# Kernel tuning notes

Hardware: AMD Instinct MI355X
Metric: run time of the kernel (lower is better)

Reference implementation:

```python
import jax, jax.numpy as jnp
import numpy as np

# Kernel offset table copied VERBATIM from the source (note the duplicated
# [-1,-1] row where [-1,1] would be expected -- we replicate the bug).
OFF = jnp.array([[-1, -1], [-1, 0], [-1, -1], [0, -1], [0, 0], [0, 1],
                 [1, -1], [1, 0], [1, 1]], dtype=jnp.float32)  # (9, 2)

T_HARD = 3.14 / 6
S_HARD = 2.0
S_RANGE = (S_HARD - 1.0 / S_HARD) / 2.0
H_VEC = jnp.array([T_HARD, S_RANGE, S_RANGE], dtype=jnp.float32)
B_VEC = jnp.array([0.0, S_RANGE, S_RANGE], dtype=jnp.float32)
BN_EPS = 1e-5


def setup_inputs() -> dict:
    key = jax.random.key(0)
    ks = jax.random.split(key, 9)
    N, C, H, W, O = 8, 128, 64, 64, 128
    return {
        "input_feat": jax.random.normal(ks[0], (N, C, H, W), jnp.float32),
        "ste_w": 0.05 * jax.random.normal(ks[1], (3, C, 1, 1), jnp.float32),
        "ste_b": 0.05 * jax.random.normal(ks[2], (3,), jnp.float32),
        "bn_gamma": 1.0 + 0.1 * jax.random.normal(ks[3], (3,), jnp.float32),
        "bn_beta": 0.1 * jax.random.normal(ks[4], (3,), jnp.float32),
        "bn_mean": 0.1 * jax.random.normal(ks[5], (3,), jnp.float32),
        "bn_var": jax.random.uniform(ks[6], (3,), jnp.float32, 0.5, 1.5),
        "dconv_w": jax.random.normal(ks[7], (O, C, 3, 3), jnp.float32) / np.sqrt(C * 9.0),
        "dconv_b": 0.05 * jax.random.normal(ks[8], (O,), jnp.float32),
    }


def _forward(input_feat, ste_w, ste_b, bn_gamma, bn_beta, bn_mean, bn_var,
             dconv_w, dconv_b):
    N, C, H, W = input_feat.shape
    O = dconv_w.shape[0]
    # --- ste: 1x1 conv -> BatchNorm (eval) -> tanh, then affine H*x + B ---
    s = jnp.einsum('nchw,oc->nohw', input_feat, ste_w[:, :, 0, 0])
    s = s + ste_b[None, :, None, None]
    scale = (bn_gamma / jnp.sqrt(bn_var + BN_EPS))
    s = (s - bn_mean[None, :, None, None]) * scale[None, :, None, None] \
        + bn_beta[None, :, None, None]
    info = jnp.tanh(s) * H_VEC[None, :, None, None] + B_VEC[None, :, None, None]
    # --- per-pixel 2x2 scaled rotation applied to kernel grid ---
    theta = info[:, 0]                  # [N,H,W]
    sin = jnp.sin(theta)
    cos = jnp.cos(theta)
    a00 = cos * info[:, 1]
    a11 = cos * info[:, 2]
    awt = jnp.stack([a00, -sin, sin, a11], axis=-1).reshape(N, H, W, 2, 2)
    offs = jnp.einsum('kd,nhwde->nkhwe', OFF, awt)   # [N,9,H,W,2]
    off_y = offs[..., 0]
    off_x = offs[..., 1]
    # --- deformable 3x3 conv, stride 1, padding 1, zero-pad bilinear ---
    k = jnp.arange(9)
    dy = (k // 3 - 1).astype(jnp.float32)  # default kernel y-offsets
    dx = (k % 3 - 1).astype(jnp.float32)
    yy = jnp.arange(H, dtype=jnp.float32)
    xx = jnp.arange(W, dtype=jnp.float32)
    y = yy[None, None, :, None] + dy[None, :, None, None] + off_y  # [N,9,H,W]
    x = xx[None, None, None, :] + dx[None, :, None, None] + off_x
    y0 = jnp.floor(y)
    x0 = jnp.floor(x)
    wy = y - y0
    wx = x - x0
    y0i = y0.astype(jnp.int32)
    x0i = x0.astype(jnp.int32)

    def gather(img, yi, xi):
        # img [C,H,W], yi/xi [9,H,W] -> [C,9,H,W], zero outside bounds
        valid = (yi >= 0) & (yi < H) & (xi >= 0) & (xi < W)
        v = img[:, jnp.clip(yi, 0, H - 1), jnp.clip(xi, 0, W - 1)]
        return v * valid[None].astype(img.dtype)

    def sample_one(img, y0i, x0i, wy, wx):
        v00 = gather(img, y0i, x0i)
        v01 = gather(img, y0i, x0i + 1)
        v10 = gather(img, y0i + 1, x0i)
        v11 = gather(img, y0i + 1, x0i + 1)
        return (v00 * ((1 - wy) * (1 - wx))[None]
                + v01 * ((1 - wy) * wx)[None]
                + v10 * (wy * (1 - wx))[None]
                + v11 * (wy * wx)[None])

    samp = jax.vmap(sample_one)(input_feat, y0i, x0i, wy, wx)  # [N,C,9,H,W]
    out = jnp.einsum('nckhw,ock->nohw', samp, dconv_w.reshape(O, C, 9))
    return out + dconv_b[None, :, None, None]


def reference(input_feat, ste_w, ste_b, bn_gamma, bn_beta, bn_mean, bn_var,
              dconv_w, dconv_b):
    return _forward(input_feat, ste_w, ste_b, bn_gamma, bn_beta, bn_mean,
                    bn_var, dconv_w, dconv_b)
```

## Files before the change

### kernel.cpp

```cpp
#include <hip/hip_runtime.h>
#include <hip/hip_bf16.h>

constexpr int kN = 8, kC = 128, kH = 64, kW = 64, kO = 128;
constexpr int kHW = kH * kW;

typedef float f32x2 __attribute__((ext_vector_type(2)));
typedef float f32x4 __attribute__((ext_vector_type(4)));
typedef short bf16x8 __attribute__((ext_vector_type(8)));
typedef unsigned short ushort8 __attribute__((ext_vector_type(8)));
typedef unsigned int u32x4 __attribute__((ext_vector_type(4)));

__device__ __forceinline__ float bf2f(unsigned short u) {
  unsigned int x = ((unsigned int)u) << 16;
  return __builtin_bit_cast(float, x);
}
__device__ __forceinline__ unsigned short f2bf(float f) {
  unsigned int b = __builtin_bit_cast(unsigned int, f);
  b += 0x7FFFu + ((b >> 16) & 1u);
  return (unsigned short)(b >> 16);
}
__device__ __forceinline__ f32x2 bf2x2(unsigned int u) {
  f32x2 r;
  r[0] = __builtin_bit_cast(float, u << 16);
  r[1] = __builtin_bit_cast(float, u & 0xFFFF0000u);
  return r;
}

#define GLOAD_LDS16(g, l)                                              \
  __builtin_amdgcn_global_load_lds(                                    \
      (const __attribute__((address_space(1))) void*)(g),              \
      (__attribute__((address_space(3))) void*)(l), 16, 0, 0)

__global__ __launch_bounds__(256) void prep_kernel(
    const float* __restrict__ inp, const float* __restrict__ ste_w,
    const float* __restrict__ ste_b, const float* __restrict__ bn_g,
    const float* __restrict__ bn_b, const float* __restrict__ bn_m,
    const float* __restrict__ bn_v, unsigned short* __restrict__ nhwc,
    float* __restrict__ prm, const float* __restrict__ dw,
    unsigned short* __restrict__ wkb) {
  const int bid = blockIdx.x;
  if (bid >= kN * kH) {
    int idx = (bid - kN * kH) * 256 + threadIdx.x;
    if (idx < 9 * kO * kC) {
      int k = idx / (kO * kC);
      int r = idx - k * (kO * kC);
      int o = r >> 7, c = r & 127;
      int c8 = c >> 3;
      int dstc = ((c8 ^ (o & 7)) << 3) | (c & 7);
      wkb[k * (kO * kC) + (o << 7) + dstc] = f2bf(dw[(o * kC + c) * 9 + k]);
    }
    return;
  }

  __shared__ __align__(16) float tile[kC * kW];
  __shared__ float part[16][3][kW];
  const int tid = threadIdx.x;
  const int nh = bid;
  const int n = nh >> 6, h = nh & 63;
  const float* base = inp + (size_t)n * kC * kHW + h * kW;

  const int w4 = tid & 15;
  const int m = tid >> 4;
  float p0[4] = {0.f, 0.f, 0.f, 0.f};
  float p1[4] = {0.f, 0.f, 0.f, 0.f};
  float p2[4] = {0.f, 0.f, 0.f, 0.f};
#pragma unroll
  for (int it = 0; it < 8; ++it) {
    const int c = m + it * 16;
    f32x4 v = *(const f32x4*)(base + c * kHW + w4 * 4);
    ((f32x4*)tile)[c * 16 + (w4 ^ ((c >> 3) & 7))] = v;
    const float s0 = ste_w[c], s1 = ste_w[kC + c], s2 = ste_w[2 * kC + c];
#pragma unroll
    for (int e = 0; e < 4; ++e) {
      p0[e] += s0 * v[e];
      p1[e] += s1 * v[e];
      p2[e] += s2 * v[e];
    }
  }
#pragma unroll
  for (int e = 0; e < 4; ++e) {
    part[m][0][w4 * 4 + e] = p0[e];
    part[m][1][w4 * 4 + e] = p1[e];
    part[m][2][w4 * 4 + e] = p2[e];
  }
  __syncthreads();

  if (tid < kW) {
    const int w = tid;
    float s0 = 0.f, s1 = 0.f, s2 = 0.f;
#pragma unroll
    for (int g = 0; g < 16; ++g) {
      s0 += part[g][0][w];
      s1 += part[g][1][w];
      s2 += part[g][2][w];
    }
    s0 = (s0 + ste_b[0] - bn_m[0]) * (bn_g[0] * rsqrtf(bn_v[0] + 1e-5f)) + bn_b[0];
    s1 = (s1 + ste_b[1] - bn_m[1]) * (bn_g[1] * rsqrtf(bn_v[1] + 1e-5f)) + bn_b[1];
    s2 = (s2 + ste_b[2] - bn_m[2]) * (bn_g[2] * rsqrtf(bn_v[2] + 1e-5f)) + bn_b[2];
    float th = tanhf(s0) * (3.14f / 6.0f);
    float i1 = tanhf(s1) * 0.75f + 0.75f;
    float i2 = tanhf(s2) * 0.75f + 0.75f;
    float sn = sinf(th), cs = cosf(th);
    prm[nh * 192 + w * 3 + 0] = cs * i1;
    prm[nh * 192 + w * 3 + 1] = sn;
    prm[nh * 192 + w * 3 + 2] = cs * i2;
  }

#pragma unroll
  for (int it = 0; it < 4; ++it) {
    int i = tid + it * 256;
    int ch = i & 15, w = i >> 4;
    int c0 = ch * 8;
    const int xw = (((w >> 2) ^ (ch & 7)) << 2) + (w & 3);
    ushort8 v;
#pragma unroll
    for (int j = 0; j < 8; ++j) v[j] = f2bf(tile[(c0 + j) * kW + xw]);
    *(ushort8*)&nhwc[((size_t)(n * kH + h) * kW + w) * kC + c0] = v;
  }
}

__global__ __launch_bounds__(512, 4) void deform_mfma_kernel(
    const unsigned short* __restrict__ nhwc,
    const unsigned short* __restrict__ wkb,
    const float* __restrict__ prm, const float* __restrict__ db,
    float* __restrict__ out) {
  __shared__ __align__(16) unsigned short As[2][32 * 128];
  __shared__ __align__(16) unsigned short Bs[2][128 * 128];

  const int tid = threadIdx.x;
  const int lane = tid & 63, wave = tid >> 6;
  const int wid = (blockIdx.x & 7) * 128 + (blockIdx.x >> 3);
  const int nh = wid >> 1;
  const int w0 = (wid & 1) << 5;
  const int n = nh >> 6, h = nh & 63;
  const unsigned short* nhwc_n = nhwc + (size_t)n * kH * kW * kC;

  const int p = tid >> 4, ch = tid & 15;
  const int cb = ch * 8;
  const float a00 = prm[nh * 192 + (w0 + p) * 3 + 0];
  const float sn  = prm[nh * 192 + (w0 + p) * 3 + 1];
  const float a11 = prm[nh * 192 + (w0 + p) * 3 + 2];

  const int mg = wave >> 2, ng = wave & 3;
  const int row = mg * 16 + (lane & 15);
  const int kq = lane >> 4;
  const int rsw = (row & 7) << 4;
  f32x4 acc[2];
  acc[0] = (f32x4){0.f, 0.f, 0.f, 0.f};
  acc[1] = (f32x4){0.f, 0.f, 0.f, 0.f};

  u32x4 aC[4];
  float wgt[4];

  auto issue_B = [&](int k, int buf) {
    const char* gk = (const char*)wkb + (size_t)k * 32768;
    char* lb = (char*)Bs[buf];
    const int wo = wave * 1024;
    const int lo16 = lane * 16;
#pragma unroll
    for (int it = 0; it < 4; ++it) {
      GLOAD_LDS16(gk + it * 8192 + wo + lo16, lb + it * 8192 + wo);
    }
  };

  auto gather_A = [&](int k) {
    const float fdy = (float)(k / 3 - 1);
    const float fdx = (float)(k % 3 - 1);
    const float o0 = fdy;
    const float o1 = (k == 2) ? -1.0f : fdx;
    float y = (float)h + fdy + o0 * a00 + o1 * sn;
    float x = (float)(w0 + p) + fdx - o0 * sn + o1 * a11;
    float y0f = floorf(y), x0f = floorf(x);
    float wy = y - y0f, wx = x - x0f;
    int y0 = (int)y0f, x0 = (int)x0f;
    bool yv0 = (unsigned)y0 < (unsigned)kH;
    bool yv1 = (unsigned)(y0 + 1) < (unsigned)kH;
    bool xv0 = (unsigned)x0 < (unsigned)kW;
    bool xv1 = (unsigned)(x0 + 1) < (unsigned)kW;
    int y0c = min(max(y0, 0), kH - 1);
    int y1c = min(max(y0 + 1, 0), kH - 1);
    int x0c = min(max(x0, 0), kW - 1);
    int x1c = min(max(x0 + 1, 0), kW - 1);
    wgt[0] = (1.f - wy) * (1.f - wx) * (yv0 && xv0 ? 1.f : 0.f);
    wgt[1] = (1.f - wy) * wx * (yv0 && xv1 ? 1.f : 0.f);
    wgt[2] = wy * (1.f - wx) * (yv1 && xv0 ? 1.f : 0.f);
    wgt[3] = wy * wx * (yv1 && xv1 ? 1.f : 0.f);
    aC[0] = *(const u32x4*)&nhwc_n[((y0c * kW) + x0c) * kC + cb];
    aC[1] = *(const u32x4*)&nhwc_n[((y0c * kW) + x1c) * kC + cb];
    aC[2] = *(const u32x4*)&nhwc_n[((y1c * kW) + x0c) * kC + cb];
    aC[3] = *(const u32x4*)&nhwc_n[((y1c * kW) + x1c) * kC + cb];
  };

  auto write_A = [&](int buf) {
    u32x4 r;
#pragma unroll
    for (int t = 0; t < 4; ++t) {
      f32x2 v = bf2x2(aC[0][t]) * wgt[0] + bf2x2(aC[1][t]) * wgt[1] +
                bf2x2(aC[2][t]) * wgt[2] + bf2x2(aC[3][t]) * wgt[3];
      __hip_bfloat162 pk = __float22bfloat162_rn(float2{v[0], v[1]});
      unsigned int bits;
      __builtin_memcpy(&bits, &pk, 4);
      r[t] = bits;
    }
    *(u32x4*)((char*)As[buf] + p * 256 + ((ch * 16) ^ ((p & 7) << 4))) = r;
  };

  issue_B(0, 0);
  gather_A(0);
  write_A(0);
  __syncthreads();

  for (int k = 0; k < 9; ++k) {
    const int cur = k & 1;
    if (k < 8) {
      gather_A(k + 1);
      issue_B(k + 1, cur ^ 1);
    }

    const char* Ab = (const char*)As[cur] + row * 256;
    const char* Bb = (const char*)Bs[cur];
#pragma unroll
    for (int ks = 0; ks < 4; ++ks) {
      const int kb = ks * 64 + kq * 16;
      bf16x8 a = *(const bf16x8*)(Ab + (kb ^ rsw));
#pragma unroll
      for (int f = 0; f < 2; ++f) {
        const int orow = (ng * 2 + f) * 16 + (lane & 15);
        bf16x8 b = *(const bf16x8*)(Bb + orow * 256 + (kb ^ ((orow & 7) << 4)));
        acc[f] = __builtin_amdgcn_mfma_f32_16x16x32_bf16(a, b, acc[f], 0, 0, 0);
      }
    }

    if (k < 8) write_A(cur ^ 1);
    __syncthreads();
  }

  const int pixb = mg * 16 + (lane >> 4) * 4;
#pragma unroll
  for (int f = 0; f < 2; ++f) {
    const int o = (ng * 2 + f) * 16 + (lane & 15);
    const float bias = db[o];
    float4 v = {acc[f][0] + bias, acc[f][1] + bias, acc[f][2] + bias,
                acc[f][3] + bias};
    *(float4*)&out[((size_t)(n * kO + o)) * kHW + h * kW + w0 + pixb] = v;
  }
}

__global__ __launch_bounds__(256) void deform_kernel_f32(
    const float* __restrict__ inp, const float* __restrict__ ste_w,
    const float* __restrict__ ste_b, const float* __restrict__ bn_g,
    const float* __restrict__ bn_b, const float* __restrict__ bn_m,
    const float* __restrict__ bn_v, const float* __restrict__ dw,
    const float* __restrict__ db, float* __restrict__ out) {
  __shared__ __align__(16) float smp[kC * 16];
  __shared__ float prm[16][3];
  const int tid = threadIdx.x;
  const int base = blockIdx.x * 16;
  const int n = base / kHW;
  const int hw = base - n * kHW;
  const int h = hw / kW;
  const int w0 = hw - h * kW;
  const float* inp_n = inp + (size_t)n * kC * kHW;

  for (int i = tid; i < kC * 16; i += 256) {
    int c = i >> 4, p = i & 15;
    smp[i] = inp_n[c * kHW + h * kW + w0 + p];
  }
  __syncthreads();
  {
    const int p = tid >> 4, cl = tid & 15;
    float a0 = 0.f, a1 = 0.f, a2 = 0.f;
#pragma unroll
    for (int i = 0; i < 8; ++i) {
      int c = cl + (i << 4);
      float v = smp[c * 16 + p];
      a0 += v * ste_w[c];
      a1 += v * ste_w[kC + c];
      a2 += v * ste_w[2 * kC + c];
    }
#pragma unroll
    for (int off = 8; off; off >>= 1) {
      a0 += __shfl_down(a0, off, 16);
      a1 += __shfl_down(a1, off, 16);
      a2 += __shfl_down(a2, off, 16);
    }
    if (cl == 0) {
      float s0 = (a0 + ste_b[0] - bn_m[0]) * (bn_g[0] * rsqrtf(bn_v[0] + 1e-5f)) + bn_b[0];
      float s1 = (a1 + ste_b[1] - bn_m[1]) * (bn_g[1] * rsqrtf(bn_v[1] + 1e-5f)) + bn_b[1];
      float s2 = (a2 + ste_b[2] - bn_m[2]) * (bn_g[2] * rsqrtf(bn_v[2] + 1e-5f)) + bn_b[2];
      float th = tanhf(s0) * (3.14f / 6.0f);
      float i1 = tanhf(s1) * 0.75f + 0.75f;
      float i2 = tanhf(s2) * 0.75f + 0.75f;
      prm[p][0] = cosf(th) * i1;
      prm[p][1] = sinf(th);
      prm[p][2] = cosf(th) * i2;
    }
  }
  const int o = tid & 127;
  const int ph = tid >> 7;
  float acc[8] = {0.f};
  for (int k = 0; k < 9; ++k) {
    __syncthreads();
    const float fdy = (float)(k / 3 - 1);
    const float fdx = (float)(k % 3 - 1);
    const float o0 = fdy;
    const float o1 = (k == 2) ? -1.0f : fdx;
    for (int i = tid; i < kC * 16; i += 256) {
      int c = i >> 4, p = i & 15;
      float a00 = prm[p][0], sn = prm[p][1], a11 = prm[p][2];
      float y = (float)h + fdy + o0 * a00 + o1 * sn;
      float x = (float)(w0 + p) + fdx - o0 * sn + o1 * a11;
      float y0f = floorf(y), x0f = floorf(x);
      float wy = y - y0f, wx = x - x0f;
      int y0 = (int)y0f, x0 = (int)x0f;
      const float* ic = inp_n + c * kHW;
      bool yv0 = (unsigned)y0 < (unsigned)kH;
      bool yv1 = (unsigned)(y0 + 1) < (unsigned)kH;
      bool xv0 = (unsigned)x0 < (unsigned)kW;
      bool xv1 = (unsigned)(x0 + 1) < (unsigned)kW;
      int y0c = min(max(y0, 0), kH - 1);
      int y1c = min(max(y0 + 1, 0), kH - 1);
      int x0c = min(max(x0, 0), kW - 1);
      int x1c = min(max(x0 + 1, 0), kW - 1);
      float v00 = (yv0 && xv0) ? ic[y0c * kW + x0c] : 0.f;
      float v01 = (yv0 && xv1) ? ic[y0c * kW + x1c] : 0.f;
      float v10 = (yv1 && xv0) ? ic[y1c * kW + x0c] : 0.f;
      float v11 = (yv1 && xv1) ? ic[y1c * kW + x1c] : 0.f;
      smp[i] = v00 * (1.f - wy) * (1.f - wx) + v01 * (1.f - wy) * wx +
               v10 * wy * (1.f - wx) + v11 * wy * wx;
    }
    __syncthreads();
    const float* wp = dw + (size_t)o * kC * 9 + k;
#pragma unroll 4
    for (int c = 0; c < kC; ++c) {
      float wv = wp[(size_t)c * 9];
      const float4 s0 = *(const float4*)&smp[c * 16 + (ph << 3)];
      const float4 s1 = *(const float4*)&smp[c * 16 + (ph << 3) + 4];
      acc[0] += wv * s0.x; acc[1] += wv * s0.y; acc[2] += wv * s0.z; acc[3] += wv * s0.w;
      acc[4] += wv * s1.x; acc[5] += wv * s1.y; acc[6] += wv * s1.z; acc[7] += wv * s1.w;
    }
  }
  const float bias = db[o];
  float* op = out + ((size_t)(n * kO + o)) * kHW + h * kW + w0 + (ph << 3);
#pragma unroll
  for (int j = 0; j < 8; ++j) op[j] = acc[j] + bias;
}

extern "C" void kernel_launch(void* const* d_in, const int* in_sizes, int n_in,
                              void* d_out, int out_size, void* d_ws, size_t ws_size,
                              hipStream_t stream) {
  const float* inp   = (const float*)d_in[0];
  const float* ste_w = (const float*)d_in[1];
  const float* ste_b = (const float*)d_in[2];
  const float* bn_g  = (const float*)d_in[3];
  const float* bn_b  = (const float*)d_in[4];
  const float* bn_m  = (const float*)d_in[5];
  const float* bn_v  = (const float*)d_in[6];
  const float* dw    = (const float*)d_in[7];
  const float* db    = (const float*)d_in[8];
  float* out = (float*)d_out;

  const size_t nhwc_bytes = (size_t)kN * kH * kW * kC * 2;
  const size_t wkb_bytes = (size_t)9 * kO * kC * 2;
  const size_t prm_bytes = (size_t)kN * kH * kW * 3 * 4;
  const size_t need = nhwc_bytes + wkb_bytes + prm_bytes;

  if (ws_size >= need) {
    unsigned short* nhwc = (unsigned short*)d_ws;
    unsigned short* wkb = (unsigned short*)((char*)d_ws + nhwc_bytes);
    float* prm = (float*)((char*)d_ws + nhwc_bytes + wkb_bytes);
    const int reorder_blocks = (9 * kO * kC + 255) / 256;
    prep_kernel<<<kN * kH + reorder_blocks, 256, 0, stream>>>(
        inp, ste_w, ste_b, bn_g, bn_b, bn_m, bn_v, nhwc, prm, dw, wkb);
    deform_mfma_kernel<<<kN * kH * 2, 512, 0, stream>>>(nhwc, wkb, prm, db, out);
  } else {
    deform_kernel_f32<<<kN * kHW / 16, 256, 0, stream>>>(
        inp, ste_w, ste_b, bn_g, bn_b, bn_m, bn_v, dw, db, out);
  }
}
```

Measured before the change: 46.86 us.

## Switch to 32x32x16 MFMA with split-K across wave pairs and LDS reduction

Each wave now owns a 32-pixel by 32-output tile and covers half of the channel dimension with the 32x32x16 bf16 MFMA, in place of two 16x16x32 tiles over the full channel range. The two partial sums are combined through LDS (reusing the B buffer) after an extra barrier, then bias is added and results are stored. This cuts LDS fragment reads per MFMA and uses the larger MFMA shape, at the cost of a reduction pass, an extra sync, and half the waves idling during the epilogue.

```diff
diff --git a/kernel.cpp b/kernel.cpp
--- a/kernel.cpp
+++ b/kernel.cpp
@@ -6,6 +6,7 @@
 
 typedef float f32x2 __attribute__((ext_vector_type(2)));
 typedef float f32x4 __attribute__((ext_vector_type(4)));
+typedef float f32x16 __attribute__((ext_vector_type(16)));
 typedef short bf16x8 __attribute__((ext_vector_type(8)));
 typedef unsigned short ushort8 __attribute__((ext_vector_type(8)));
 typedef unsigned int u32x4 __attribute__((ext_vector_type(4)));
@@ -141,13 +142,17 @@
   const float sn  = prm[nh * 192 + (w0 + p) * 3 + 1];
   const float a11 = prm[nh * 192 + (w0 + p) * 3 + 2];
 
-  const int mg = wave >> 2, ng = wave & 3;
-  const int row = mg * 16 + (lane & 15);
-  const int kq = lane >> 4;
-  const int rsw = (row & 7) << 4;
-  f32x4 acc[2];
-  acc[0] = (f32x4){0.f, 0.f, 0.f, 0.f};
-  acc[1] = (f32x4){0.f, 0.f, 0.f, 0.f};
+  const int q = wave >> 1;
+  const int khalf = wave & 1;
+  const int arow = lane & 31;
+  const int brow = q * 32 + (lane & 31);
+  const int koff = (lane >> 5) * 16;
+  const int aswz = (arow & 7) << 4;
+  const int bswz = (brow & 7) << 4;
+
+  f32x16 acc;
+#pragma unroll
+  for (int j = 0; j < 16; ++j) acc[j] = 0.f;
 
   u32x4 aC[4];
   float wgt[4];
@@ -217,32 +222,39 @@
       issue_B(k + 1, cur ^ 1);
     }
 
-    const char* Ab = (const char*)As[cur] + row * 256;
-    const char* Bb = (const char*)Bs[cur];
-#pragma unroll
-    for (int ks = 0; ks < 4; ++ks) {
-      const int kb = ks * 64 + kq * 16;
-      bf16x8 a = *(const bf16x8*)(Ab + (kb ^ rsw));
-#pragma unroll
-      for (int f = 0; f < 2; ++f) {
-        const int orow = (ng * 2 + f) * 16 + (lane & 15);
-        bf16x8 b = *(const bf16x8*)(Bb + orow * 256 + (kb ^ ((orow & 7) << 4)));
-        acc[f] = __builtin_amdgcn_mfma_f32_16x16x32_bf16(a, b, acc[f], 0, 0, 0);
-      }
+    const char* Ab = (const char*)As[cur] + arow * 256;
+    const char* Bb = (const char*)Bs[cur] + brow * 256;
+#pragma unroll
+    for (int c = 0; c < 4; ++c) {
+      const int kb = (khalf * 4 + c) * 32 + koff;
+      bf16x8 a = *(const bf16x8*)(Ab + (kb ^ aswz));
+      bf16x8 b = *(const bf16x8*)(Bb + (kb ^ bswz));
+      acc = __builtin_amdgcn_mfma_f32_32x32x16_bf16(a, b, acc, 0, 0, 0);
     }
 
     if (k < 8) write_A(cur ^ 1);
     __syncthreads();
   }
 
-  const int pixb = mg * 16 + (lane >> 4) * 4;
-#pragma unroll
-  for (int f = 0; f < 2; ++f) {
-    const int o = (ng * 2 + f) * 16 + (lane & 15);
+  float* red = (float*)&Bs[0][0];
+  if (khalf == 1) {
+#pragma unroll
+    for (int j = 0; j < 16; ++j) red[q * 1024 + j * 64 + lane] = acc[j];
+  }
+  __syncthreads();
+  if (khalf == 0) {
+#pragma unroll
+    for (int j = 0; j < 16; ++j) acc[j] += red[q * 1024 + j * 64 + lane];
+    const int o = q * 32 + (lane & 31);
     const float bias = db[o];
-    float4 v = {acc[f][0] + bias, acc[f][1] + bias, acc[f][2] + bias,
-                acc[f][3] + bias};
-    *(float4*)&out[((size_t)(n * kO + o)) * kHW + h * kW + w0 + pixb] = v;
+    float* obase = out + ((size_t)(n * kO + o)) * kHW + h * kW + w0 +
+                   4 * (lane >> 5);
+#pragma unroll
+    for (int qq = 0; qq < 4; ++qq) {
+      float4 v = {acc[4 * qq + 0] + bias, acc[4 * qq + 1] + bias,
+                  acc[4 * qq + 2] + bias, acc[4 * qq + 3] + bias};
+      *(float4*)&obase[8 * qq] = v;
+    }
   }
 }
 
```

Result: no change. 46.62 us (-0.5%).
